# Kernel tuning notes

Measured on AMD Instinct MI355X. Metric: run time of the kernel, lower is better.

The kernel has to match this reference:

```python
import jax, jax.numpy as jnp
import numpy as np

T, B, I, H = 1024, 64, 512, 512


def setup_inputs() -> dict:
    key = jax.random.key(0)
    ks = jax.random.split(key, 6)
    s = 1.0 / np.sqrt(H).astype(np.float32)
    x = jax.random.normal(ks[0], (T, B, I), jnp.float32)
    lengths = jax.random.randint(ks[1], (B,), 1, T + 1)
    # descending-sorted ragged lengths, max length equals T (as module assumes)
    lengths = jnp.sort(lengths)[::-1].at[0].set(T)
    w_ih = jax.random.normal(ks[2], (3 * H, I), jnp.float32) * s
    w_hh = jax.random.normal(ks[3], (3 * H, H), jnp.float32) * s
    b_ih = jax.random.normal(ks[4], (3 * H,), jnp.float32) * s
    b_hh = jax.random.normal(ks[5], (3 * H,), jnp.float32) * s
    return {"x": x, "batch_lengths": lengths, "w_ih": w_ih, "w_hh": w_hh,
            "b_ih": b_ih, "b_hh": b_hh}


def reference(x, batch_lengths, w_ih, w_hh, b_ih, b_hh):
    Tn, Bn, _ = x.shape
    Hn = w_hh.shape[1]
    # Precompute all input-side gate projections in one big GEMM: [T,B,3H]
    gx = jnp.einsum('tbi,gi->tbg', x, w_ih) + b_ih
    # Ragged mask: timestep t is active for sequence b iff t < length[b]
    mask = (jnp.arange(Tn)[:, None] < batch_lengths[None, :])[..., None]  # [T,B,1]
    h0 = jnp.zeros((Bn, Hn), x.dtype)

    def step(h, inp):
        gx_t, m = inp  # gx_t: [B,3H], m: [B,1]
        gh = h @ w_hh.T + b_hh  # [B,3H]
        xr, xz, xn = jnp.split(gx_t, 3, axis=-1)
        hr, hz, hn = jnp.split(gh, 3, axis=-1)
        r = jax.nn.sigmoid(xr + hr)
        z = jax.nn.sigmoid(xz + hz)
        n = jnp.tanh(xn + r * hn)
        h_new = (1.0 - z) * n + z * h  # torch GRUCell update
        h_next = jnp.where(m, h_new, h)  # hold state past sequence end
        out_t = jnp.where(m, h_new, jnp.zeros_like(h_new))  # output stays zero-padded
        return h_next, out_t

    h_last, output = jax.lax.scan(step, h0, (gx, mask))
    return output, h_last[None]  # ([T,B,H], [1,B,H])
```

## Files before the change

### kernel.cpp

```cpp
#include <hip/hip_runtime.h>

#define T_STEPS 1024
#define BATCH   64
#define IN_F    512
#define HID     512
#define G3      1536
#define M_ROWS  (T_STEPS * BATCH)

#define NSLICE  16
#define NGROUP  16
#define SPG     4
#define HB_U64  (2 * NGROUP * SPG * 256)

typedef _Float16 v8h  __attribute__((ext_vector_type(8)));
typedef float    v4f  __attribute__((ext_vector_type(4)));

#define BM 64
#define BN 128
#define BK 32
#define LDP 40

__global__ __launch_bounds__(256) void gemm_gx(
    const float* __restrict__ X, const float* __restrict__ W,
    const float* __restrict__ bias, _Float16* __restrict__ C) {
  __shared__ _Float16 As[BM][LDP];
  __shared__ _Float16 Bs[BN][LDP];
  const int tid  = threadIdx.x;
  const int lane = tid & 63;
  const int wave = tid >> 6;
  const int m0 = blockIdx.y * BM;
  const int n0 = blockIdx.x * BN;

  v4f acc[8];
#pragma unroll
  for (int i = 0; i < 8; ++i) acc[i] = (v4f){0.f, 0.f, 0.f, 0.f};

  const int srow  = tid >> 2;
  const int kpart = (tid & 3) * 8;
  const int fr = lane & 15;
  const int ko = (lane >> 4) * 8;

  for (int kc = 0; kc < IN_F; kc += BK) {
    {
      const float* s = X + (size_t)(m0 + srow) * IN_F + kc + kpart;
      float4 a = *(const float4*)s;
      float4 b = *(const float4*)(s + 4);
      v8h o = {(_Float16)a.x, (_Float16)a.y, (_Float16)a.z, (_Float16)a.w,
               (_Float16)b.x, (_Float16)b.y, (_Float16)b.z, (_Float16)b.w};
      *(v8h*)&As[srow][kpart] = o;
    }
#pragma unroll
    for (int r = 0; r < 2; ++r) {
      const float* s = W + (size_t)(n0 + r * 64 + srow) * IN_F + kc + kpart;
      float4 a = *(const float4*)s;
      float4 b = *(const float4*)(s + 4);
      v8h o = {(_Float16)a.x, (_Float16)a.y, (_Float16)a.z, (_Float16)a.w,
               (_Float16)b.x, (_Float16)b.y, (_Float16)b.z, (_Float16)b.w};
      *(v8h*)&Bs[r * 64 + srow][kpart] = o;
    }
    __syncthreads();
    v8h af = *(const v8h*)&As[wave * 16 + fr][ko];
#pragma unroll
    for (int nt = 0; nt < 8; ++nt) {
      v8h bf = *(const v8h*)&Bs[nt * 16 + fr][ko];
      acc[nt] = __builtin_amdgcn_mfma_f32_16x16x32_f16(af, bf, acc[nt], 0, 0, 0);
    }
    __syncthreads();
  }

  const int rq = lane >> 4;
#pragma unroll
  for (int nt = 0; nt < 8; ++nt) {
    const int gcol = n0 + nt * 16 + fr;
    const float bv = bias[gcol];
#pragma unroll
    for (int r = 0; r < 4; ++r) {
      const int grow = m0 + wave * 16 + rq * 4 + r;
      C[(size_t)grow * G3 + gcol] = (_Float16)(acc[nt][r] + bv);
    }
  }
}

__global__ void zero_hbuf(unsigned long long* h) {
  const int i = blockIdx.x * 256 + threadIdx.x;
  if (i < HB_U64) h[i] = 0ull;
}

__global__ __launch_bounds__(192, 2) void gru_scan2(
    const _Float16* __restrict__ gx, const float* __restrict__ whh,
    const int* __restrict__ lens, const float* __restrict__ bhh,
    float* __restrict__ out, unsigned long long* hbuf) {
  const int bid   = blockIdx.x;
  const int slice = bid >> 4;
  const int grp   = bid & 15;
  const int b0  = grp * SPG;
  const int tid  = threadIdx.x;
  const int lane = tid & 63;
  const int w    = tid >> 6;

  __shared__ __align__(16) _Float16 h16[16 * 520];
  __shared__ __align__(16) float ghl[3 * 32 * 4];

  for (int i = tid; i < 16 * 520 / 2; i += 192) ((unsigned*)h16)[i] = 0u;

  v8h bw0[16], bw1[16];
  {
    const int r15 = lane & 15;
    const int k8  = (lane >> 4) * 8;
    const float* p0 = whh + (size_t)(w * 512 + slice * 32 + r15) * HID + k8;
    const float* p1 = p0 + 16 * HID;
#pragma unroll
    for (int kt = 0; kt < 16; ++kt) {
      float4 a = *(const float4*)(p0 + kt * 32);
      float4 b = *(const float4*)(p0 + kt * 32 + 4);
      bw0[kt] = (v8h){(_Float16)a.x, (_Float16)a.y, (_Float16)a.z, (_Float16)a.w,
                      (_Float16)b.x, (_Float16)b.y, (_Float16)b.z, (_Float16)b.w};
      float4 c = *(const float4*)(p1 + kt * 32);
      float4 d = *(const float4*)(p1 + kt * 32 + 4);
      bw1[kt] = (v8h){(_Float16)c.x, (_Float16)c.y, (_Float16)c.z, (_Float16)c.w,
                      (_Float16)d.x, (_Float16)d.y, (_Float16)d.z, (_Float16)d.w};
    }
  }

  const int eseq = tid >> 4;
  const int ec0  = (tid & 15) * 2;
  const int ej   = slice * 32 + ec0;
  float hr0 = 0.f, hr1 = 0.f;
  float br0 = 0, br1 = 0, bz0 = 0, bz1 = 0, bn0 = 0, bn1 = 0;
  int mylen = 0;
  unsigned pg0 = 0, pg1 = 0, pg2 = 0;
  if (tid < 64) {
    br0 = bhh[ej];        br1 = bhh[ej + 1];
    bz0 = bhh[ej + 512];  bz1 = bhh[ej + 513];
    bn0 = bhh[ej + 1024]; bn1 = bhh[ej + 1025];
    mylen = lens[b0 + eseq];
    const _Float16* gxr = gx + ((size_t)0 * BATCH + b0 + eseq) * G3 + ej;
    pg0 = *(const unsigned*)gxr;
    pg1 = *(const unsigned*)(gxr + 512);
    pg2 = *(const unsigned*)(gxr + 1024);
  }
  const int glen = max(max(lens[b0], lens[b0 + 1]), max(lens[b0 + 2], lens[b0 + 3]));
  __syncthreads();

  const int arow = lane & 15;
  const int ak   = (lane >> 4) * 8;
  const _Float16* hbase = &h16[arow * 520 + ak];

  int ii[6]; int nn = 0;
  for (int i = tid; i < SPG * 256; i += 192) { ii[nn] = i; ++nn; }

  for (int t = 0; t < glen; ++t) {
    v4f acc0 = (v4f){0.f, 0.f, 0.f, 0.f};
    v4f acc1 = (v4f){0.f, 0.f, 0.f, 0.f};
#pragma unroll
    for (int kt = 0; kt < 16; ++kt) {
      v8h af = *(const v8h*)(hbase + kt * 32);
      acc0 = __builtin_amdgcn_mfma_f32_16x16x32_f16(af, bw0[kt], acc0, 0, 0, 0);
      acc1 = __builtin_amdgcn_mfma_f32_16x16x32_f16(af, bw1[kt], acc1, 0, 0, 0);
    }
    if (lane < 16) {
      *(v4f*)&ghl[(w * 32 + lane) * 4]      = acc0;
      *(v4f*)&ghl[(w * 32 + 16 + lane) * 4] = acc1;
    }
    __syncthreads();

    if (tid < 64) {
      const float ar0 = ghl[(0 * 32 + ec0) * 4 + eseq], ar1 = ghl[(0 * 32 + ec0 + 1) * 4 + eseq];
      const float az0 = ghl[(1 * 32 + ec0) * 4 + eseq], az1 = ghl[(1 * 32 + ec0 + 1) * 4 + eseq];
      const float an0 = ghl[(2 * 32 + ec0) * 4 + eseq], an1 = ghl[(2 * 32 + ec0 + 1) * 4 + eseq];
      union { unsigned u; _Float16 h[2]; } g0, g1, g2, pk;
      g0.u = pg0; g1.u = pg1; g2.u = pg2;
      float* o = out + (size_t)t * (BATCH * HID) + (size_t)(b0 + eseq) * HID + ej;
      if (t < mylen) {
        const float r0 = 1.f / (1.f + __expf(-((float)g0.h[0] + ar0 + br0)));
        const float z0 = 1.f / (1.f + __expf(-((float)g1.h[0] + az0 + bz0)));
        const float p0 = (float)g2.h[0] + r0 * (an0 + bn0);
        const float n0v = 1.f - 2.f / (__expf(2.f * p0) + 1.f);
        hr0 = (1.f - z0) * n0v + z0 * hr0;
        const float r1 = 1.f / (1.f + __expf(-((float)g0.h[1] + ar1 + br1)));
        const float z1 = 1.f / (1.f + __expf(-((float)g1.h[1] + az1 + bz1)));
        const float p1 = (float)g2.h[1] + r1 * (an1 + bn1);
        const float n1v = 1.f - 2.f / (__expf(2.f * p1) + 1.f);
        hr1 = (1.f - z1) * n1v + z1 * hr1;
        o[0] = hr0; o[1] = hr1;
      } else {
        o[0] = 0.f; o[1] = 0.f;
      }
      pk.h[0] = (_Float16)hr0; pk.h[1] = (_Float16)hr1;
      const unsigned long long pv =
          ((unsigned long long)(unsigned)(t + 1) << 32) | pk.u;
      const size_t di = (size_t)((((t + 1) & 1) * NGROUP + grp) * SPG + eseq) * 256
                        + slice * 16 + (tid & 15);
      __hip_atomic_store(hbuf + di, pv, __ATOMIC_RELAXED,
                         __HIP_MEMORY_SCOPE_AGENT);
      const int tn = (t + 1 < glen) ? t + 1 : t;
      const _Float16* gxr = gx + ((size_t)tn * BATCH + b0 + eseq) * G3 + ej;
      pg0 = *(const unsigned*)gxr;
      pg1 = *(const unsigned*)(gxr + 512);
      pg2 = *(const unsigned*)(gxr + 1024);
    }

    {
      const unsigned long long* src = hbuf
          + (size_t)(((t + 1) & 1) * NGROUP + grp) * (SPG * 256);
      const unsigned want = (unsigned)(t + 1);
      unsigned long long got[6];
      unsigned pend = (1u << nn) - 1u;
      while (pend) {
#pragma unroll
        for (int j = 0; j < 6; ++j)
          if (j < nn && (pend & (1u << j)))
            got[j] = __hip_atomic_load(src + ii[j], __ATOMIC_RELAXED,
                                       __HIP_MEMORY_SCOPE_AGENT);
#pragma unroll
        for (int j = 0; j < 6; ++j)
          if (j < nn && (pend & (1u << j)) &&
              (unsigned)(got[j] >> 32) >= want) {
            const int sq = ii[j] >> 8, jj = ii[j] & 255;
            *(unsigned*)&h16[sq * 520 + jj * 2] = (unsigned)got[j];
            pend &= ~(1u << j);
          }
        if (pend) __builtin_amdgcn_s_sleep(1);
      }
    }
    __syncthreads();
  }

  if (tid < 64) {
    for (int t = glen; t < T_STEPS; ++t) {
      float* o = out + (size_t)t * (BATCH * HID) + (size_t)(b0 + eseq) * HID + ej;
      o[0] = 0.f; o[1] = 0.f;
    }
    float* hl = out + (size_t)T_STEPS * BATCH * HID + (size_t)(b0 + eseq) * HID + ej;
    hl[0] = hr0; hl[1] = hr1;
  }
}

extern "C" void kernel_launch(void* const* d_in, const int* in_sizes, int n_in,
                              void* d_out, int out_size, void* d_ws, size_t ws_size,
                              hipStream_t stream) {
  const float* x    = (const float*)d_in[0];
  const int*   lens = (const int*)d_in[1];
  const float* w_ih = (const float*)d_in[2];
  const float* w_hh = (const float*)d_in[3];
  const float* b_ih = (const float*)d_in[4];
  const float* b_hh = (const float*)d_in[5];
  float* out = (float*)d_out;

  _Float16* gxbuf = (_Float16*)d_ws;
  unsigned long long* hbuf = (unsigned long long*)(gxbuf + (size_t)M_ROWS * G3);

  zero_hbuf<<<dim3((HB_U64 + 255) / 256), dim3(256), 0, stream>>>(hbuf);
  gemm_gx<<<dim3(G3 / BN, M_ROWS / BM), dim3(256), 0, stream>>>(x, w_ih, b_ih, gxbuf);
  gru_scan2<<<dim3(NSLICE * NGROUP), dim3(192), 0, stream>>>(
      gxbuf, w_hh, lens, b_hh, out, hbuf);
}
```

Before: 2.436 ms.

## Restructure GRU scan into 32 persistent blocks with two interleaved batch chunks

Replaces the 256-block scan, where each block handled 4 sequences and a 32-column slice, with 32 blocks that each own 32 sequences split into two 16-row chunks. The chunks are processed in alternating phases so one chunk's h exchange latency overlaps with the other's MFMA and gate work. It also prefetches the next chunk's hbuf words before the barrier and splits the MFMA accumulation into two chains. Zeroing of padded output rows moves to a separate kernel. Fewer blocks means much less parallelism per step and more serialized work per block, which may offset the gain from overlapping the cross-block synchronization.

```diff
diff --git a/kernel.cpp b/kernel.cpp
--- a/kernel.cpp
+++ b/kernel.cpp
@@ -7,10 +7,7 @@
 #define G3      1536
 #define M_ROWS  (T_STEPS * BATCH)
 
-#define NSLICE  16
-#define NGROUP  16
-#define SPG     4
-#define HB_U64  (2 * NGROUP * SPG * 256)
+#define HB_U64  (2 * 4 * 16 * 256)
 
 typedef _Float16 v8h  __attribute__((ext_vector_type(8)));
 typedef float    v4f  __attribute__((ext_vector_type(4)));
@@ -86,25 +83,159 @@
   if (i < HB_U64) h[i] = 0ull;
 }
 
-__global__ __launch_bounds__(192, 2) void gru_scan2(
+__global__ __launch_bounds__(256) void zero_out_tail(const int* __restrict__ lens,
+                                                     float* __restrict__ out) {
+  __shared__ int slen[BATCH];
+  if (threadIdx.x < BATCH) slen[threadIdx.x] = lens[threadIdx.x];
+  __syncthreads();
+  for (int row = blockIdx.x; row < T_STEPS * BATCH; row += gridDim.x) {
+    const int t = row >> 6;
+    const int b = row & 63;
+    if (t < slen[b]) continue;
+    float2* dst = (float2*)(out + (size_t)row * HID);
+    dst[threadIdx.x] = make_float2(0.f, 0.f);
+  }
+}
+
+static __device__ __forceinline__ void wg_barrier() {
+  asm volatile("s_waitcnt lgkmcnt(0)" ::: "memory");
+  __builtin_amdgcn_s_barrier();
+  asm volatile("" ::: "memory");
+}
+
+#define PHASE(C)                                                               \
+  {                                                                            \
+    const int chunk = set * 2 + C;                                             \
+                   \
+    if (t > 0) {                                                               \
+      const unsigned want = (unsigned)t;                                       \
+      const unsigned long long* src =                                          \
+          hbuf + (((size_t)((t & 1) * 4 + chunk)) << 12);                      \
+      unsigned pend = 0xffffu;                                                 \
+      while (true) {                                                           \
+        unsigned np = 0u;                                                      \
+        _Pragma("unroll") for (int k = 0; k < 16; ++k) {                       \
+          if (pend & (1u << k)) {                                              \
+            if ((unsigned)(got[k] >> 32) >= want) {                            \
+              *(unsigned*)&h16f[C * (16 * 520) + k * 520 + tid * 2] =          \
+                  (unsigned)got[k];                                            \
+            } else np |= (1u << k);                                            \
+          }                                                                    \
+        }                                                                      \
+        if (!np) break;                                                        \
+        __builtin_amdgcn_s_sleep(1);                                           \
+        _Pragma("unroll") for (int k = 0; k < 16; ++k) {                       \
+          if (np & (1u << k))                                                  \
+            got[k] = __hip_atomic_load(src + k * 256 + tid, __ATOMIC_RELAXED,  \
+                                       __HIP_MEMORY_SCOPE_AGENT);              \
+        }                                                                      \
+        pend = np;                                                             \
+      }                                                                        \
+    }                                                                          \
+                \
+    {                                                                          \
+      int tn, cn;                                                              \
+      if (C == 0) {                                                            \
+        if (t < glen1) { tn = t; cn = 1; } else { tn = t + 1; cn = 0; }        \
+      } else {                                                                 \
+        if (t + 1 < glen0) { tn = t + 1; cn = 0; } else { tn = t + 1; cn = 1; }\
+      }                                                                        \
+      const int gl = (cn == 0) ? glen0 : glen1;                                \
+      if (tn >= 1 && tn < gl) {                                                \
+        const unsigned long long* srcn =                                       \
+            hbuf + (((size_t)((tn & 1) * 4 + set * 2 + cn)) << 12);            \
+        _Pragma("unroll") for (int k = 0; k < 16; ++k)                         \
+          got[k] = __hip_atomic_load(srcn + k * 256 + tid, __ATOMIC_RELAXED,   \
+                                     __HIP_MEMORY_SCOPE_AGENT);               \
+      }                                                                        \
+    }                                                                          \
+    wg_barrier();     \
+           \
+    if (w < 3) {                                                               \
+      const _Float16* hb = h16f + C * (16 * 520) + arow * 520 + ak;            \
+      v4f a0a = (v4f){0.f, 0.f, 0.f, 0.f}, a0b = a0a, a1a = a0a, a1b = a0a;    \
+      _Pragma("unroll") for (int kt = 0; kt < 8; ++kt) {                       \
+        v8h af = *(const v8h*)(hb + kt * 32);                                  \
+        a0a = __builtin_amdgcn_mfma_f32_16x16x32_f16(af, bw0[kt], a0a, 0,0,0); \
+        a1a = __builtin_amdgcn_mfma_f32_16x16x32_f16(af, bw1[kt], a1a, 0,0,0); \
+      }                                                                        \
+      _Pragma("unroll") for (int kt = 8; kt < 16; ++kt) {                      \
+        v8h af = *(const v8h*)(hb + kt * 32);                                  \
+        a0b = __builtin_amdgcn_mfma_f32_16x16x32_f16(af, bw0[kt], a0b, 0,0,0); \
+        a1b = __builtin_amdgcn_mfma_f32_16x16x32_f16(af, bw1[kt], a1b, 0,0,0); \
+      }                                                                        \
+      v4f acc0 = a0a + a0b;                                                    \
+      v4f acc1 = a1a + a1b;                                                    \
+      const int col = lane & 15;                                               \
+      const int sg  = lane >> 4;                                               \
+      *(v4f*)&ghl[(w * 32 + col) * 20 + sg * 4]      = acc0;                   \
+      *(v4f*)&ghl[(w * 32 + 16 + col) * 20 + sg * 4] = acc1;                   \
+    }                                                                          \
+    wg_barrier();                                 \
+                     \
+    {                                                                          \
+      const float ar0 = ghl[(0 * 32 + ec0) * 20 + eseq];                       \
+      const float ar1 = ghl[(0 * 32 + ec0 + 1) * 20 + eseq];                   \
+      const float az0 = ghl[(1 * 32 + ec0) * 20 + eseq];                       \
+      const float az1 = ghl[(1 * 32 + ec0 + 1) * 20 + eseq];                   \
+      const float an0 = ghl[(2 * 32 + ec0) * 20 + eseq];                       \
+      const float an1 = ghl[(2 * 32 + ec0 + 1) * 20 + eseq];                   \
+      union { unsigned u; _Float16 h[2]; } g0, g1, g2;                         \
+      g0.u = pg[C][0]; g1.u = pg[C][1]; g2.u = pg[C][2];                       \
+      const int bq = (C == 0) ? b0 : b1;                                       \
+      float h0 = hr[C][0], h1 = hr[C][1];                                      \
+      if (t < mylen[C]) {                                                      \
+        const float r0 = 1.f / (1.f + __expf(-((float)g0.h[0] + ar0 + br0)));  \
+        const float z0 = 1.f / (1.f + __expf(-((float)g1.h[0] + az0 + bz0)));  \
+        const float p0 = (float)g2.h[0] + r0 * (an0 + bn0);                    \
+        const float n0v = 1.f - 2.f / (__expf(2.f * p0) + 1.f);                \
+        h0 = (1.f - z0) * n0v + z0 * h0;                                       \
+        const float r1 = 1.f / (1.f + __expf(-((float)g0.h[1] + ar1 + br1)));  \
+        const float z1 = 1.f / (1.f + __expf(-((float)g1.h[1] + az1 + bz1)));  \
+        const float p1 = (float)g2.h[1] + r1 * (an1 + bn1);                    \
+        const float n1v = 1.f - 2.f / (__expf(2.f * p1) + 1.f);                \
+        h1 = (1.f - z1) * n1v + z1 * h1;                                       \
+        hr[C][0] = h0; hr[C][1] = h1;                                          \
+        float* o = out + (size_t)t * (BATCH * HID) + (size_t)bq * HID + ej;    \
+        *(float2*)o = make_float2(h0, h1);                                     \
+      }                                                                        \
+      union { unsigned u; _Float16 h[2]; } pk;                                 \
+      pk.h[0] = (_Float16)h0; pk.h[1] = (_Float16)h1;                          \
+      const unsigned long long pv =                                            \
+          ((unsigned long long)(unsigned)(t + 1) << 32) | pk.u;                \
+      const size_t di = (((size_t)(((t + 1) & 1) * 4 + chunk)) << 12) +        \
+                        (size_t)eseq * 256 + slice * 16 + (tid & 15);          \
+      __hip_atomic_store(hbuf + di, pv, __ATOMIC_RELAXED,                      \
+                         __HIP_MEMORY_SCOPE_AGENT);                            \
+      const int gcl = (C == 0) ? glen0 : glen1;                                \
+      const int tn2 = (t + 1 < gcl) ? t + 1 : t;                               \
+      const _Float16* gxr = gx + ((size_t)tn2 * BATCH + bq) * G3 + ej;         \
+      pg[C][0] = *(const unsigned*)gxr;                                        \
+      pg[C][1] = *(const unsigned*)(gxr + 512);                                \
+      pg[C][2] = *(const unsigned*)(gxr + 1024);                               \
+    }                                                                          \
+  }
+
+__global__ __launch_bounds__(256, 1) void gru_scan3(
     const _Float16* __restrict__ gx, const float* __restrict__ whh,
     const int* __restrict__ lens, const float* __restrict__ bhh,
     float* __restrict__ out, unsigned long long* hbuf) {
   const int bid   = blockIdx.x;
-  const int slice = bid >> 4;
-  const int grp   = bid & 15;
-  const int b0  = grp * SPG;
+  const int slice = bid & 15;
+  const int set   = bid >> 4;
   const int tid  = threadIdx.x;
   const int lane = tid & 63;
   const int w    = tid >> 6;
 
-  __shared__ __align__(16) _Float16 h16[16 * 520];
-  __shared__ __align__(16) float ghl[3 * 32 * 4];
-
-  for (int i = tid; i < 16 * 520 / 2; i += 192) ((unsigned*)h16)[i] = 0u;
+  __shared__ __align__(16) _Float16 h16f[2 * 16 * 520];
+  __shared__ __align__(16) float ghl[3 * 32 * 20];
+  __shared__ int sgl[2];
+
+  if (tid == 0) { sgl[0] = 0; sgl[1] = 0; }
+  for (int i = tid; i < (2 * 16 * 520) / 2; i += 256) ((unsigned*)h16f)[i] = 0u;
 
   v8h bw0[16], bw1[16];
-  {
+  if (w < 3) {
     const int r15 = lane & 15;
     const int k8  = (lane >> 4) * 8;
     const float* p0 = whh + (size_t)(w * 512 + slice * 32 + r15) * HID + k8;
@@ -115,9 +246,9 @@
       float4 b = *(const float4*)(p0 + kt * 32 + 4);
       bw0[kt] = (v8h){(_Float16)a.x, (_Float16)a.y, (_Float16)a.z, (_Float16)a.w,
                       (_Float16)b.x, (_Float16)b.y, (_Float16)b.z, (_Float16)b.w};
-      float4 c = *(const float4*)(p1 + kt * 32);
-      float4 d = *(const float4*)(p1 + kt * 32 + 4);
-      bw1[kt] = (v8h){(_Float16)c.x, (_Float16)c.y, (_Float16)c.z, (_Float16)c.w,
+      float4 cc = *(const float4*)(p1 + kt * 32);
+      float4 d  = *(const float4*)(p1 + kt * 32 + 4);
+      bw1[kt] = (v8h){(_Float16)cc.x, (_Float16)cc.y, (_Float16)cc.z, (_Float16)cc.w,
                       (_Float16)d.x, (_Float16)d.y, (_Float16)d.z, (_Float16)d.w};
     }
   }
@@ -125,114 +256,47 @@
   const int eseq = tid >> 4;
   const int ec0  = (tid & 15) * 2;
   const int ej   = slice * 32 + ec0;
-  float hr0 = 0.f, hr1 = 0.f;
-  float br0 = 0, br1 = 0, bz0 = 0, bz1 = 0, bn0 = 0, bn1 = 0;
-  int mylen = 0;
-  unsigned pg0 = 0, pg1 = 0, pg2 = 0;
-  if (tid < 64) {
-    br0 = bhh[ej];        br1 = bhh[ej + 1];
-    bz0 = bhh[ej + 512];  bz1 = bhh[ej + 513];
-    bn0 = bhh[ej + 1024]; bn1 = bhh[ej + 1025];
-    mylen = lens[b0 + eseq];
-    const _Float16* gxr = gx + ((size_t)0 * BATCH + b0 + eseq) * G3 + ej;
-    pg0 = *(const unsigned*)gxr;
-    pg1 = *(const unsigned*)(gxr + 512);
-    pg2 = *(const unsigned*)(gxr + 1024);
-  }
-  const int glen = max(max(lens[b0], lens[b0 + 1]), max(lens[b0 + 2], lens[b0 + 3]));
+  const int b0   = set * 32 + 2 * eseq;
+  const int b1   = b0 + 1;
+
+  float hr[2][2] = {{0.f, 0.f}, {0.f, 0.f}};
+  const float br0 = bhh[ej];        const float br1 = bhh[ej + 1];
+  const float bz0 = bhh[ej + 512];  const float bz1 = bhh[ej + 513];
+  const float bn0 = bhh[ej + 1024]; const float bn1 = bhh[ej + 1025];
+  const int mylen[2] = { lens[b0], lens[b1] };
+  unsigned pg[2][3];
+  {
+    const _Float16* g0p = gx + (size_t)b0 * G3 + ej;
+    pg[0][0] = *(const unsigned*)g0p;
+    pg[0][1] = *(const unsigned*)(g0p + 512);
+    pg[0][2] = *(const unsigned*)(g0p + 1024);
+    const _Float16* g1p = gx + (size_t)b1 * G3 + ej;
+    pg[1][0] = *(const unsigned*)g1p;
+    pg[1][1] = *(const unsigned*)(g1p + 512);
+    pg[1][2] = *(const unsigned*)(g1p + 1024);
+  }
   __syncthreads();
+  atomicMax(&sgl[0], mylen[0]);
+  atomicMax(&sgl[1], mylen[1]);
+  __syncthreads();
+  const int glen0 = sgl[0];
+  const int glen1 = sgl[1];
+  const int gmax  = (glen0 > glen1) ? glen0 : glen1;
 
   const int arow = lane & 15;
   const int ak   = (lane >> 4) * 8;
-  const _Float16* hbase = &h16[arow * 520 + ak];
-
-  int ii[6]; int nn = 0;
-  for (int i = tid; i < SPG * 256; i += 192) { ii[nn] = i; ++nn; }
-
-  for (int t = 0; t < glen; ++t) {
-    v4f acc0 = (v4f){0.f, 0.f, 0.f, 0.f};
-    v4f acc1 = (v4f){0.f, 0.f, 0.f, 0.f};
-#pragma unroll
-    for (int kt = 0; kt < 16; ++kt) {
-      v8h af = *(const v8h*)(hbase + kt * 32);
-      acc0 = __builtin_amdgcn_mfma_f32_16x16x32_f16(af, bw0[kt], acc0, 0, 0, 0);
-      acc1 = __builtin_amdgcn_mfma_f32_16x16x32_f16(af, bw1[kt], acc1, 0, 0, 0);
-    }
-    if (lane < 16) {
-      *(v4f*)&ghl[(w * 32 + lane) * 4]      = acc0;
-      *(v4f*)&ghl[(w * 32 + 16 + lane) * 4] = acc1;
-    }
-    __syncthreads();
-
-    if (tid < 64) {
-      const float ar0 = ghl[(0 * 32 + ec0) * 4 + eseq], ar1 = ghl[(0 * 32 + ec0 + 1) * 4 + eseq];
-      const float az0 = ghl[(1 * 32 + ec0) * 4 + eseq], az1 = ghl[(1 * 32 + ec0 + 1) * 4 + eseq];
-      const float an0 = ghl[(2 * 32 + ec0) * 4 + eseq], an1 = ghl[(2 * 32 + ec0 + 1) * 4 + eseq];
-      union { unsigned u; _Float16 h[2]; } g0, g1, g2, pk;
-      g0.u = pg0; g1.u = pg1; g2.u = pg2;
-      float* o = out + (size_t)t * (BATCH * HID) + (size_t)(b0 + eseq) * HID + ej;
-      if (t < mylen) {
-        const float r0 = 1.f / (1.f + __expf(-((float)g0.h[0] + ar0 + br0)));
-        const float z0 = 1.f / (1.f + __expf(-((float)g1.h[0] + az0 + bz0)));
-        const float p0 = (float)g2.h[0] + r0 * (an0 + bn0);
-        const float n0v = 1.f - 2.f / (__expf(2.f * p0) + 1.f);
-        hr0 = (1.f - z0) * n0v + z0 * hr0;
-        const float r1 = 1.f / (1.f + __expf(-((float)g0.h[1] + ar1 + br1)));
-        const float z1 = 1.f / (1.f + __expf(-((float)g1.h[1] + az1 + bz1)));
-        const float p1 = (float)g2.h[1] + r1 * (an1 + bn1);
-        const float n1v = 1.f - 2.f / (__expf(2.f * p1) + 1.f);
-        hr1 = (1.f - z1) * n1v + z1 * hr1;
-        o[0] = hr0; o[1] = hr1;
-      } else {
-        o[0] = 0.f; o[1] = 0.f;
-      }
-      pk.h[0] = (_Float16)hr0; pk.h[1] = (_Float16)hr1;
-      const unsigned long long pv =
-          ((unsigned long long)(unsigned)(t + 1) << 32) | pk.u;
-      const size_t di = (size_t)((((t + 1) & 1) * NGROUP + grp) * SPG + eseq) * 256
-                        + slice * 16 + (tid & 15);
-      __hip_atomic_store(hbuf + di, pv, __ATOMIC_RELAXED,
-                         __HIP_MEMORY_SCOPE_AGENT);
-      const int tn = (t + 1 < glen) ? t + 1 : t;
-      const _Float16* gxr = gx + ((size_t)tn * BATCH + b0 + eseq) * G3 + ej;
-      pg0 = *(const unsigned*)gxr;
-      pg1 = *(const unsigned*)(gxr + 512);
-      pg2 = *(const unsigned*)(gxr + 1024);
-    }
-
-    {
-      const unsigned long long* src = hbuf
-          + (size_t)(((t + 1) & 1) * NGROUP + grp) * (SPG * 256);
-      const unsigned want = (unsigned)(t + 1);
-      unsigned long long got[6];
-      unsigned pend = (1u << nn) - 1u;
-      while (pend) {
-#pragma unroll
-        for (int j = 0; j < 6; ++j)
-          if (j < nn && (pend & (1u << j)))
-            got[j] = __hip_atomic_load(src + ii[j], __ATOMIC_RELAXED,
-                                       __HIP_MEMORY_SCOPE_AGENT);
-#pragma unroll
-        for (int j = 0; j < 6; ++j)
-          if (j < nn && (pend & (1u << j)) &&
-              (unsigned)(got[j] >> 32) >= want) {
-            const int sq = ii[j] >> 8, jj = ii[j] & 255;
-            *(unsigned*)&h16[sq * 520 + jj * 2] = (unsigned)got[j];
-            pend &= ~(1u << j);
-          }
-        if (pend) __builtin_amdgcn_s_sleep(1);
-      }
-    }
-    __syncthreads();
-  }
-
-  if (tid < 64) {
-    for (int t = glen; t < T_STEPS; ++t) {
-      float* o = out + (size_t)t * (BATCH * HID) + (size_t)(b0 + eseq) * HID + ej;
-      o[0] = 0.f; o[1] = 0.f;
-    }
-    float* hl = out + (size_t)T_STEPS * BATCH * HID + (size_t)(b0 + eseq) * HID + ej;
-    hl[0] = hr0; hl[1] = hr1;
+
+  unsigned long long got[16];
+
+  for (int t = 0; t < gmax; ++t) {
+    if (t < glen0) PHASE(0)
+    if (t < glen1) PHASE(1)
+  }
+
+  {
+    float* hl = out + (size_t)T_STEPS * BATCH * HID;
+    *(float2*)(hl + (size_t)b0 * HID + ej) = make_float2(hr[0][0], hr[0][1]);
+    *(float2*)(hl + (size_t)b1 * HID + ej) = make_float2(hr[1][0], hr[1][1]);
   }
 }
 
@@ -251,7 +315,7 @@
   unsigned long long* hbuf = (unsigned long long*)(gxbuf + (size_t)M_ROWS * G3);
 
   zero_hbuf<<<dim3((HB_U64 + 255) / 256), dim3(256), 0, stream>>>(hbuf);
+  zero_out_tail<<<dim3(2048), dim3(256), 0, stream>>>(lens, out);
   gemm_gx<<<dim3(G3 / BN, M_ROWS / BM), dim3(256), 0, stream>>>(x, w_ih, b_ih, gxbuf);
-  gru_scan2<<<dim3(NSLICE * NGROUP), dim3(192), 0, stream>>>(
-      gxbuf, w_hh, lens, b_hh, out, hbuf);
-}
+  gru_scan3<<<dim3(32), dim3(256), 0, stream>>>(gxbuf, w_hh, lens, b_hh, out, hbuf);
+}
```

Result: slower. 5.263 ms (+116.1%).
